# Kernel tuning notes

Measured on AMD Instinct MI355X. Metric: run time of the kernel, lower is better.

Reference implementation:

```python
import jax, jax.numpy as jnp
import numpy as np

B, N, M, D, NHEAD, FF, C, K = 2, 16384, 2048, 256, 8, 512, 50, 3
HID = 128          # embed/pos hidden
HEAD_HID = 256     # seg head hidden
L = 4              # depth
EPS = 1e-5


def setup_inputs() -> dict:
    key = jax.random.key(0)
    ks = jax.random.split(key, 32)
    g = lambda i, shape: jax.random.normal(ks[i], shape, dtype=jnp.float32) * 0.02
    z = lambda shape: jnp.zeros(shape, jnp.float32)
    o = lambda shape: jnp.ones(shape, jnp.float32)
    return {
        "xyz": jax.random.normal(ks[0], (B, N, 3), dtype=jnp.float32),
        "embed_w1": g(1, (3, HID)), "embed_b1": z((HID,)),
        "embed_w2": g(2, (HID, D)), "embed_b2": z((D,)),
        "pos_w1": g(3, (3, HID)), "pos_b1": z((HID,)),
        "pos_w2": g(4, (HID, D)), "pos_b2": z((D,)),
        "Wq": g(5, (L, D, D)), "bq": z((L, D)),
        "Wk": g(6, (L, D, D)), "bk": z((L, D)),
        "Wv": g(7, (L, D, D)), "bv": z((L, D)),
        "Wo": g(8, (L, D, D)), "bo": z((L, D)),
        "ln1_s": o((L, D)), "ln1_b": z((L, D)),
        "W1": g(9, (L, D, FF)), "b1": z((L, FF)),
        "W2": g(10, (L, FF, D)), "b2": z((L, D)),
        "ln2_s": o((L, D)), "ln2_b": z((L, D)),
        "head_w1": g(11, (D, HEAD_HID)), "head_b1": z((HEAD_HID,)),
        "head_w2": g(12, (HEAD_HID, C)), "head_b2": z((C,)),
    }


def _ln(x, s, b):
    m = x.mean(-1, keepdims=True)
    v = ((x - m) ** 2).mean(-1, keepdims=True)
    return (x - m) / jnp.sqrt(v + EPS) * s + b


def reference(xyz, embed_w1, embed_b1, embed_w2, embed_b2,
              pos_w1, pos_b1, pos_w2, pos_b2,
              Wq, bq, Wk, bk, Wv, bv, Wo, bo, ln1_s, ln1_b,
              W1, b1, W2, b2, ln2_s, ln2_b,
              head_w1, head_b1, head_w2, head_b2):
    # deterministic token subsample (replaces randperm stub): strided pick of M points
    stride = N // M
    tok = xyz[:, ::stride, :][:, :M]                                  # [B,M,3]
    # per-point embed + learned positional encoding
    x = jax.nn.relu(tok @ embed_w1 + embed_b1) @ embed_w2 + embed_b2  # [B,M,D]
    x = x + jax.nn.relu(tok @ pos_w1 + pos_b1) @ pos_w2 + pos_b2
    dh = D // NHEAD
    scale = 1.0 / jnp.sqrt(jnp.float32(dh))

    def layer(x, p):
        wq, bq_, wk, bk_, wv, bv_, wo, bo_, l1s, l1b, w1, b1_, w2, b2_, l2s, l2b = p
        # pre-norm MHSA
        y = _ln(x, l1s, l1b)
        q = (y @ wq + bq_).reshape(B, M, NHEAD, dh)
        k = (y @ wk + bk_).reshape(B, M, NHEAD, dh)
        v = (y @ wv + bv_).reshape(B, M, NHEAD, dh)
        att = jax.nn.softmax(jnp.einsum('bqhd,bkhd->bhqk', q, k) * scale, axis=-1)
        o = jnp.einsum('bhqk,bkhd->bqhd', att, v).reshape(B, M, D)
        x = x + o @ wo + bo_
        # pre-norm FFN (gelu, exact erf as in torch)
        y = _ln(x, l2s, l2b)
        x = x + jax.nn.gelu(y @ w1 + b1_, approximate=False) @ w2 + b2_
        return x, None

    x, _ = jax.lax.scan(layer, x, (Wq, bq, Wk, bk, Wv, bv, Wo, bo,
                                   ln1_s, ln1_b, W1, b1, W2, b2, ln2_s, ln2_b))
    logits_tok = jax.nn.relu(x @ head_w1 + head_b1) @ head_w2 + head_b2  # [B,M,C]

    # kNN propagation N->M: dist^2 = |q|^2 + |k|^2 - 2 q.k, topk smallest
    q2 = (xyz ** 2).sum(-1)[..., None]            # [B,N,1]
    k2 = (tok ** 2).sum(-1)[:, None, :]           # [B,1,M]
    dist = q2 + k2 - 2.0 * jnp.einsum('bnd,bmd->bnm', xyz, tok)
    dist = jax.lax.stop_gradient(jnp.maximum(dist, 0.0))
    idx = jax.lax.top_k(-dist, K)[1]              # [B,N,K]
    logits_nk = logits_tok[jnp.arange(B)[:, None, None], idx]  # [B,N,K,C]
    return logits_nk.mean(axis=2)                 # [B,N,C]
```

## Files before the change

### kernel.cpp

```cpp
#include <hip/hip_runtime.h>
#include <hip/hip_bf16.h>
#include <math.h>

#define B_ 2
#define N_ 16384
#define M_ 2048
#define D_ 256
#define NHEAD_ 8
#define DH_ 32
#define FF_ 512
#define C_ 50
#define HID_ 128
#define HHID_ 256
#define L_ 4
#define EPS_ 1e-5f
#define TOK_ (B_*M_)
#define QSCALE_ 0.25507604155757994f

typedef short short8 __attribute__((ext_vector_type(8)));
typedef float f32x4 __attribute__((ext_vector_type(4)));

__device__ __forceinline__ short f2bf(float f) {
  union { float f; unsigned u; } c; c.f = f;
  unsigned u = c.u;
  unsigned r = (u + 0x7FFFu + ((u >> 16) & 1u)) >> 16;
  return (short)r;
}
__device__ __forceinline__ unsigned pack2bf(float a, float b) {
  return ((unsigned)(unsigned short)f2bf(a)) | (((unsigned)(unsigned short)f2bf(b)) << 16);
}
__device__ __forceinline__ float fast_exp2(float x) {
  float r;
  asm("v_exp_f32 %0, %1" : "=v"(r) : "v"(x));
  return r;
}
__device__ __forceinline__ unsigned cvt_pk_bf16(float lo, float hi) {
  unsigned r;
  asm("v_cvt_pk_bf16_f32 %0, %1, %2" : "=v"(r) : "v"(lo), "v"(hi));
  return r;
}

__global__ __launch_bounds__(128) void embed_kernel(
    const float* __restrict__ xyz,
    const float* __restrict__ ew1, const float* __restrict__ eb1,
    const float* __restrict__ ew2, const float* __restrict__ eb2,
    const float* __restrict__ pw1, const float* __restrict__ pb1,
    const float* __restrict__ pw2, const float* __restrict__ pb2,
    float* __restrict__ x) {
  int t = blockIdx.x;
  int b = t / M_, m = t % M_;
  const float* p = xyz + ((size_t)b * N_ + (size_t)m * 8) * 3;
  float t0 = p[0], t1 = p[1], t2 = p[2];
  __shared__ float he[HID_], hp[HID_];
  int j = threadIdx.x;
  {
    float a = fmaf(t0, ew1[j], fmaf(t1, ew1[HID_ + j], fmaf(t2, ew1[2 * HID_ + j], eb1[j])));
    he[j] = fmaxf(a, 0.f);
    float c = fmaf(t0, pw1[j], fmaf(t1, pw1[HID_ + j], fmaf(t2, pw1[2 * HID_ + j], pb1[j])));
    hp[j] = fmaxf(c, 0.f);
  }
  __syncthreads();
  for (int d = j; d < D_; d += HID_) {
    float acc = eb2[d] + pb2[d];
    for (int k = 0; k < HID_; ++k) {
      acc = fmaf(he[k], ew2[k * D_ + d], acc);
      acc = fmaf(hp[k], pw2[k * D_ + d], acc);
    }
    x[(size_t)t * D_ + d] = acc;
  }
}

__global__ __launch_bounds__(256) void ln_kernel(
    const float* __restrict__ x, const float* __restrict__ s,
    const float* __restrict__ bb, float* __restrict__ y) {
  int r = blockIdx.x * 4 + (threadIdx.x >> 6);
  int t = threadIdx.x & 63;
  const float4* xr = (const float4*)(x + (size_t)r * D_);
  float4 v = xr[t];
  float sum = v.x + v.y + v.z + v.w;
  #pragma unroll
  for (int o = 1; o < 64; o <<= 1) sum += __shfl_xor(sum, o, 64);
  float mean = sum * (1.f / D_);
  float dx = v.x - mean, dy = v.y - mean, dz = v.z - mean, dw = v.w - mean;
  float vs = dx * dx + dy * dy + dz * dz + dw * dw;
  #pragma unroll
  for (int o = 1; o < 64; o <<= 1) vs += __shfl_xor(vs, o, 64);
  float inv = 1.0f / sqrtf(vs * (1.f / D_) + EPS_);
  float4 sv = ((const float4*)s)[t];
  float4 bv = ((const float4*)bb)[t];
  float4 out;
  out.x = dx * inv * sv.x + bv.x;
  out.y = dy * inv * sv.y + bv.y;
  out.z = dz * inv * sv.z + bv.z;
  out.w = dw * inv * sv.w + bv.w;
  ((float4*)(y + (size_t)r * D_))[t] = out;
}

template <int ACT, int RES>
__global__ __launch_bounds__(256) void gemm_kernel(
    const float* __restrict__ A, const float* __restrict__ W,
    const float* __restrict__ bias, const float* __restrict__ R,
    float* __restrict__ Cc, int K, int Ncols) {
  __shared__ float As[16][68];
  __shared__ float Ws[16][68];
  int m0 = blockIdx.y * 64;
  int n0 = blockIdx.x * 64;
  int tid = threadIdx.x;
  int tx = tid & 15, ty = tid >> 4;
  float acc[4][4] = {};
  for (int kk = 0; kk < K; kk += 16) {
    for (int i = tid; i < 64 * 16; i += 256) {
      int mm = i >> 4, kq = i & 15;
      As[kq][mm] = A[(size_t)(m0 + mm) * K + kk + kq];
    }
    for (int i = tid; i < 16 * 64; i += 256) {
      int kq = i >> 6, nn = i & 63;
      int n = n0 + nn;
      Ws[kq][nn] = (n < Ncols) ? W[(size_t)(kk + kq) * Ncols + n] : 0.f;
    }
    __syncthreads();
    #pragma unroll
    for (int kq = 0; kq < 16; ++kq) {
      float a[4], w[4];
      #pragma unroll
      for (int i = 0; i < 4; ++i) a[i] = As[kq][ty * 4 + i];
      #pragma unroll
      for (int jj = 0; jj < 4; ++jj) w[jj] = Ws[kq][tx * 4 + jj];
      #pragma unroll
      for (int i = 0; i < 4; ++i)
        #pragma unroll
        for (int jj = 0; jj < 4; ++jj) acc[i][jj] = fmaf(a[i], w[jj], acc[i][jj]);
    }
    __syncthreads();
  }
  #pragma unroll
  for (int i = 0; i < 4; ++i) {
    int m = m0 + ty * 4 + i;
    #pragma unroll
    for (int jj = 0; jj < 4; ++jj) {
      int n = n0 + tx * 4 + jj;
      if (n >= Ncols) continue;
      float v = acc[i][jj] + bias[n];
      if (ACT == 1) v = fmaxf(v, 0.f);
      else if (ACT == 2) v = 0.5f * v * (1.f + erff(v * 0.70710678118654752f));
      if (RES) v += R[(size_t)m * Ncols + n];
      Cc[(size_t)m * Ncols + n] = v;
    }
  }
}

template <int ACT, int RES>
__device__ __forceinline__ void gemm_body(
    const float* __restrict__ A, const float* __restrict__ W,
    const float* __restrict__ bias, const float* __restrict__ R,
    float* __restrict__ Cc, short* __restrict__ out16, float oscale,
    int K, int Ncols, int m0, int n0) {
  __shared__ short As[32][40];
  __shared__ short Bs[64][40];
  int tid = threadIdx.x;
  int w = tid >> 6, l = tid & 63;
  int lq = l & 15, lg = l >> 4;
  int wr = (w & 1) * 16, wc = (w >> 1) * 32;
  int ar = tid >> 3, ak = (tid & 7) * 4;
  int wn = tid & 63, wk = (tid >> 6) * 8;
  f32x4 acc0 = {0.f, 0.f, 0.f, 0.f};
  f32x4 acc1 = {0.f, 0.f, 0.f, 0.f};
  for (int kk = 0; kk < K; kk += 32) {
    __syncthreads();
    {
      float4 a4 = *(const float4*)(A + (size_t)(m0 + ar) * K + kk + ak);
      uint2 au;
      au.x = pack2bf(a4.x, a4.y);
      au.y = pack2bf(a4.z, a4.w);
      *(uint2*)&As[ar][ak] = au;
      const float* wp = W + (size_t)(kk + wk) * Ncols + n0 + wn;
      float w0 = wp[0];
      float w1 = wp[(size_t)Ncols];
      float w2 = wp[2 * (size_t)Ncols];
      float w3 = wp[3 * (size_t)Ncols];
      float w4 = wp[4 * (size_t)Ncols];
      float w5 = wp[5 * (size_t)Ncols];
      float w6 = wp[6 * (size_t)Ncols];
      float w7 = wp[7 * (size_t)Ncols];
      uint4 wu;
      wu.x = pack2bf(w0, w1); wu.y = pack2bf(w2, w3);
      wu.z = pack2bf(w4, w5); wu.w = pack2bf(w6, w7);
      *(uint4*)&Bs[wn][wk] = wu;
    }
    __syncthreads();
    short8 af = *(short8*)&As[wr + lq][lg * 8];
    short8 b0 = *(short8*)&Bs[wc + lq][lg * 8];
    short8 b1 = *(short8*)&Bs[wc + 16 + lq][lg * 8];
    acc0 = __builtin_amdgcn_mfma_f32_16x16x32_bf16(af, b0, acc0, 0, 0, 0);
    acc1 = __builtin_amdgcn_mfma_f32_16x16x32_bf16(af, b1, acc1, 0, 0, 0);
  }
  int row = m0 + wr + lg * 4;
  #pragma unroll
  for (int r = 0; r < 4; ++r) {
    #pragma unroll
    for (int fj = 0; fj < 2; ++fj) {
      int col = n0 + wc + fj * 16 + lq;
      float v = (fj ? acc1[r] : acc0[r]) + bias[col];
      if (ACT == 1) v = fmaxf(v, 0.f);
      else if (ACT == 2) v = 0.5f * v * (1.f + erff(v * 0.70710678118654752f));
      if (RES) v += R[(size_t)(row + r) * Ncols + col];
      if (out16) out16[(size_t)(row + r) * Ncols + col] = f2bf(v * oscale);
      else Cc[(size_t)(row + r) * Ncols + col] = v;
    }
  }
}

template <int ACT, int RES>
__global__ __launch_bounds__(256) void gemm_mfma(
    const float* __restrict__ A, const float* __restrict__ W,
    const float* __restrict__ bias, const float* __restrict__ R,
    float* __restrict__ Cc, int K, int Ncols) {
  gemm_body<ACT, RES>(A, W, bias, R, Cc, nullptr, 1.f, K, Ncols, blockIdx.y * 32, blockIdx.x * 64);
}

__global__ __launch_bounds__(256) void qkv_mfma(
    const float* __restrict__ A,
    const float* __restrict__ Wq, const float* __restrict__ Wk, const float* __restrict__ Wv,
    const float* __restrict__ bq, const float* __restrict__ bk, const float* __restrict__ bv,
    short* __restrict__ q16, short* __restrict__ k16, float* __restrict__ vb) {
  int sel = blockIdx.x >> 2;
  int n0 = (blockIdx.x & 3) << 6;
  const float* W = sel == 0 ? Wq : (sel == 1 ? Wk : Wv);
  const float* bb = sel == 0 ? bq : (sel == 1 ? bk : bv);
  short* out16 = sel == 0 ? q16 : (sel == 1 ? k16 : nullptr);
  float oscale = sel == 0 ? QSCALE_ : 1.f;
  gemm_body<0, 0>(A, W, bb, nullptr, vb, out16, oscale, D_, D_, blockIdx.y * 32, n0);
}

__global__ __launch_bounds__(256) void vtrans_kernel(
    const float* __restrict__ vb, short* __restrict__ vt16) {
  int bid = blockIdx.x;
  int mt = bid & 31;
  int h = (bid >> 5) & 7;
  int b = bid >> 8;
  __shared__ short ts[64][34];
  int m0 = mt * 64;
  int tid = threadIdx.x;
  int mm = tid >> 2, dd = (tid & 3) * 8;
  const float* vp = vb + (size_t)(b * M_ + m0 + mm) * D_ + h * DH_ + dd;
  float4 a0 = ((const float4*)vp)[0];
  float4 a1 = ((const float4*)vp)[1];
  ts[mm][dd + 0] = f2bf(a0.x); ts[mm][dd + 1] = f2bf(a0.y);
  ts[mm][dd + 2] = f2bf(a0.z); ts[mm][dd + 3] = f2bf(a0.w);
  ts[mm][dd + 4] = f2bf(a1.x); ts[mm][dd + 5] = f2bf(a1.y);
  ts[mm][dd + 6] = f2bf(a1.z); ts[mm][dd + 7] = f2bf(a1.w);
  __syncthreads();
  int d = tid >> 3, mc = (tid & 7) * 8;
  short8 r;
  #pragma unroll
  for (int j = 0; j < 8; ++j) r[j] = ts[mc + j][d];
  *(short8*)&vt16[(size_t)((b * NHEAD_ + h) * DH_ + d) * M_ + m0 + mc] = r;
}

#define KSTR 40
#define VSTR 72
#define PSTR 72
__global__ __launch_bounds__(256) void attn_mfma_kernel(
    const short* __restrict__ q16, const short* __restrict__ k16,
    const short* __restrict__ vt16, float* __restrict__ po, float* __restrict__ pl) {
  __shared__ short Ks[64][KSTR];
  __shared__ short Vt[32][VSTR];
  __shared__ short Ps[4][16][PSTR];
  int bid = blockIdx.x;
  int half = bid & 1;
  int qt = (bid >> 1) & 31;
  int h  = (bid >> 6) & 7;
  int b  = bid >> 9;
  int tid = threadIdx.x;
  int w  = tid >> 6;
  int l  = tid & 63;
  int lq = l & 15;
  int lg = l >> 4;

  short8 qf = *(const short8*)&q16[(size_t)(b * M_ + qt * 64 + w * 16 + lq) * D_ + h * DH_ + lg * 8];

  float l_i = 0.f;
  f32x4 o0 = {0.f, 0.f, 0.f, 0.f};
  f32x4 o1 = {0.f, 0.f, 0.f, 0.f};
  int srow = tid >> 2, scol = (tid & 3) * 8;
  int vd = tid >> 3, vm = (tid & 7) * 8;
  const short* kp = k16 + (size_t)(b * M_ + half * 1024 + srow) * D_ + h * DH_ + scol;
  const short* vp = vt16 + (size_t)((b * NHEAD_ + h) * DH_ + vd) * M_ + half * 1024 + vm;

  for (int kt = 0; kt < 16; ++kt) {
    __syncthreads();
    *(short8*)&Ks[srow][scol] = *(const short8*)(kp + (size_t)(kt * 64) * D_);
    *(short8*)&Vt[vd][vm]     = *(const short8*)(vp + kt * 64);
    __syncthreads();
    f32x4 st[4];
    #pragma unroll
    for (int t = 0; t < 4; ++t) {
      short8 kf = *(short8*)&Ks[t * 16 + lq][lg * 8];
      f32x4 z = {0.f, 0.f, 0.f, 0.f};
      st[t] = __builtin_amdgcn_mfma_f32_16x16x32_bf16(kf, qf, z, 0, 0, 0);
    }
    #pragma unroll
    for (int t = 0; t < 4; ++t)
      #pragma unroll
      for (int r2 = 0; r2 < 4; ++r2) {
        st[t][r2] = fast_exp2(st[t][r2]);
        l_i += st[t][r2];
      }
    {
      unsigned* pw = (unsigned*)&Ps[w][lq][0];
      #pragma unroll
      for (int t = 0; t < 4; ++t) {
        uint2 pk;
        pk.x = cvt_pk_bf16(st[t][0], st[t][1]);
        pk.y = cvt_pk_bf16(st[t][2], st[t][3]);
        *(uint2*)(pw + t * 8 + lg * 2) = pk;
      }
    }
    #pragma unroll
    for (int c = 0; c < 2; ++c) {
      short8 pf = *(short8*)&Ps[w][lq][c * 32 + lg * 8];
      short8 v0 = *(short8*)&Vt[lq][c * 32 + lg * 8];
      short8 v1 = *(short8*)&Vt[16 + lq][c * 32 + lg * 8];
      o0 = __builtin_amdgcn_mfma_f32_16x16x32_bf16(v0, pf, o0, 0, 0, 0);
      o1 = __builtin_amdgcn_mfma_f32_16x16x32_bf16(v1, pf, o1, 0, 0, 0);
    }
  }
  l_i += __shfl_xor(l_i, 16, 64);
  l_i += __shfl_xor(l_i, 32, 64);
  int f = (b * NHEAD_ + h) * M_ + qt * 64 + w * 16 + lq;
  float* pp = po + ((size_t)half * (16 * M_) + f) * 32;
  #pragma unroll
  for (int r2 = 0; r2 < 4; ++r2) pp[lg * 4 + r2] = o0[r2];
  #pragma unroll
  for (int r2 = 0; r2 < 4; ++r2) pp[16 + lg * 4 + r2] = o1[r2];
  if (lg == 0) pl[half * (16 * M_) + f] = l_i;
}

__global__ __launch_bounds__(256) void attn_combine(
    const float* __restrict__ po, const float* __restrict__ pl,
    float* __restrict__ o) {
  int idx = blockIdx.x * 256 + threadIdx.x;
  int f = idx >> 3, dq = (idx & 7) * 4;
  float inv = 1.f / (pl[f] + pl[16 * M_ + f]);
  const float4 a = *(const float4*)&po[(size_t)f * 32 + dq];
  const float4 c = *(const float4*)&po[(size_t)(16 * M_ + f) * 32 + dq];
  int b = f >> 14, h = (f >> 11) & 7, m = f & (M_ - 1);
  float4 r;
  r.x = (a.x + c.x) * inv;
  r.y = (a.y + c.y) * inv;
  r.z = (a.z + c.z) * inv;
  r.w = (a.w + c.w) * inv;
  *(float4*)&o[(size_t)(b * M_ + m) * D_ + h * DH_ + dq] = r;
}

__global__ __launch_bounds__(512) void knn_kernel(
    const float* __restrict__ xyz, const float* __restrict__ lt,
    float* __restrict__ out) {
  __shared__ float4 tok[2056];
  int b = blockIdx.x >> 8;
  int q0 = (blockIdx.x & 255) << 6;
  int tid = threadIdx.x;
  for (int i = tid; i < M_; i += 512) {
    const float* tp = xyz + ((size_t)b * N_ + (size_t)i * 8) * 3;
    float a = tp[0], bb = tp[1], cc = tp[2];
    tok[i + (i >> 8)] = make_float4(a, bb, cc, a * a + bb * bb + cc * cc);
  }
  __syncthreads();
  int qi = tid >> 3, sl = tid & 7;
  int n = q0 + qi;
  const float* qp = xyz + ((size_t)b * N_ + n) * 3;
  float qx = qp[0], qy = qp[1], qz = qp[2];
  float q2 = qx * qx + qy * qy + qz * qz;
  float dd0 = INFINITY, dd1 = INFINITY, dd2 = INFINITY;
  int ii0 = 0, ii1 = 0, ii2 = 0;
  const float4* cp = &tok[sl * 257];
  int mb = sl << 8;
  #pragma unroll 4
  for (int j = 0; j < 256; ++j) {
    float4 t = cp[j];
    float dot = fmaf(qx, t.x, fmaf(qy, t.y, qz * t.z));
    float d = fmaxf(q2 + t.w - 2.f * dot, 0.f);
    if (d < dd2) {
      int m = mb + j;
      if (d < dd1) {
        dd2 = dd1; ii2 = ii1;
        if (d < dd0) { dd1 = dd0; ii1 = ii0; dd0 = d; ii0 = m; }
        else         { dd1 = d;  ii1 = m; }
      } else         { dd2 = d;  ii2 = m; }
    }
  }
  auto insT = [&](float d, int i) {
    if (d < dd2 || (d == dd2 && i < ii2)) {
      if (d < dd1 || (d == dd1 && i < ii1)) {
        dd2 = dd1; ii2 = ii1;
        if (d < dd0 || (d == dd0 && i < ii0)) { dd1 = dd0; ii1 = ii0; dd0 = d; ii0 = i; }
        else { dd1 = d; ii1 = i; }
      } else { dd2 = d; ii2 = i; }
    }
  };
  #pragma unroll
  for (int off = 1; off < 8; off <<= 1) {
    float pd0 = __shfl_xor(dd0, off, 64); int pi0 = __shfl_xor(ii0, off, 64);
    float pd1 = __shfl_xor(dd1, off, 64); int pi1 = __shfl_xor(ii1, off, 64);
    float pd2 = __shfl_xor(dd2, off, 64); int pi2 = __shfl_xor(ii2, off, 64);
    insT(pd0, pi0); insT(pd1, pi1); insT(pd2, pi2);
  }
  const float* l0 = lt + ((size_t)b * M_ + ii0) * C_;
  const float* l1 = lt + ((size_t)b * M_ + ii1) * C_;
  const float* l2 = lt + ((size_t)b * M_ + ii2) * C_;
  float* op = out + ((size_t)b * N_ + n) * C_;
  for (int cc = sl; cc < C_; cc += 8)
    op[cc] = (l0[cc] + l1[cc] + l2[cc]) * (1.f / 3.f);
}

extern "C" void kernel_launch(void* const* d_in, const int* in_sizes, int n_in,
                              void* d_out, int out_size, void* d_ws, size_t ws_size,
                              hipStream_t stream) {
  const float* xyz  = (const float*)d_in[0];
  const float* ew1  = (const float*)d_in[1];
  const float* eb1  = (const float*)d_in[2];
  const float* ew2  = (const float*)d_in[3];
  const float* eb2  = (const float*)d_in[4];
  const float* pw1  = (const float*)d_in[5];
  const float* pb1  = (const float*)d_in[6];
  const float* pw2  = (const float*)d_in[7];
  const float* pb2  = (const float*)d_in[8];
  const float* Wq   = (const float*)d_in[9];
  const float* bq   = (const float*)d_in[10];
  const float* Wk   = (const float*)d_in[11];
  const float* bk   = (const float*)d_in[12];
  const float* Wv   = (const float*)d_in[13];
  const float* bv   = (const float*)d_in[14];
  const float* Wo   = (const float*)d_in[15];
  const float* bo   = (const float*)d_in[16];
  const float* ln1s = (const float*)d_in[17];
  const float* ln1b = (const float*)d_in[18];
  const float* W1   = (const float*)d_in[19];
  const float* b1   = (const float*)d_in[20];
  const float* W2   = (const float*)d_in[21];
  const float* b2   = (const float*)d_in[22];
  const float* ln2s = (const float*)d_in[23];
  const float* ln2b = (const float*)d_in[24];
  const float* hw1  = (const float*)d_in[25];
  const float* hb1  = (const float*)d_in[26];
  const float* hw2  = (const float*)d_in[27];
  const float* hb2  = (const float*)d_in[28];
  float* out = (float*)d_out;

  float* x  = (float*)d_ws;
  float* y  = x  + (size_t)TOK_ * D_;
  float* qb = y  + (size_t)TOK_ * D_;
  float* kb = qb + (size_t)TOK_ * D_;
  float* vb = kb + (size_t)TOK_ * D_;
  float* ob = vb + (size_t)TOK_ * D_;
  float* ff = ob + (size_t)TOK_ * D_;
  float* lt = ff + (size_t)TOK_ * FF_;

  short* qb16 = (short*)qb;
  short* kb16 = qb16 + (size_t)TOK_ * D_;
  short* vt16 = (short*)kb;
  float* po = ff;
  float* pl = lt;

  embed_kernel<<<TOK_, 128, 0, stream>>>(xyz, ew1, eb1, ew2, eb2, pw1, pb1, pw2, pb2, x);

  dim3 gQKV(12, TOK_ / 32);
  dim3 gD(D_ / 64, TOK_ / 32);
  dim3 gF(FF_ / 64, TOK_ / 32);
  for (int l = 0; l < L_; ++l) {
    const float* wq = Wq + (size_t)l * D_ * D_;
    const float* wk = Wk + (size_t)l * D_ * D_;
    const float* wv = Wv + (size_t)l * D_ * D_;
    const float* wo = Wo + (size_t)l * D_ * D_;
    ln_kernel<<<TOK_ / 4, 256, 0, stream>>>(x, ln1s + l * D_, ln1b + l * D_, y);
    qkv_mfma<<<gQKV, 256, 0, stream>>>(y, wq, wk, wv, bq + l * D_, bk + l * D_, bv + l * D_, qb16, kb16, vb);
    vtrans_kernel<<<512, 256, 0, stream>>>(vb, vt16);
    attn_mfma_kernel<<<1024, 256, 0, stream>>>(qb16, kb16, vt16, po, pl);
    attn_combine<<<1024, 256, 0, stream>>>(po, pl, ob);
    gemm_mfma<0, 1><<<gD, 256, 0, stream>>>(ob, wo, bo + l * D_, x, x, D_, D_);
    ln_kernel<<<TOK_ / 4, 256, 0, stream>>>(x, ln2s + l * D_, ln2b + l * D_, y);
    gemm_mfma<2, 0><<<gF, 256, 0, stream>>>(y, W1 + (size_t)l * D_ * FF_, b1 + l * FF_, nullptr, ff, D_, FF_);
    gemm_mfma<0, 1><<<gD, 256, 0, stream>>>(ff, W2 + (size_t)l * FF_ * D_, b2 + l * D_, x, x, FF_, D_);
  }
  gemm_mfma<1, 0><<<dim3(HHID_ / 64, TOK_ / 32), 256, 0, stream>>>(x, hw1, hb1, nullptr, y, D_, HHID_);
  gemm_kernel<0, 0><<<dim3(1, TOK_ / 64), 256, 0, stream>>>(y, hw2, hb2, nullptr, lt, HHID_, C_);
  knn_kernel<<<512, 512, 0, stream>>>(xyz, lt, out);
}
```

Before: 436.6 us.

## Split attention keys into four partitions and add dedicated head2 kernel

```diff
diff --git a/kernel.cpp b/kernel.cpp
--- a/kernel.cpp
+++ b/kernel.cpp
@@ -96,57 +96,24 @@
   ((float4*)(y + (size_t)r * D_))[t] = out;
 }
 
-template <int ACT, int RES>
-__global__ __launch_bounds__(256) void gemm_kernel(
-    const float* __restrict__ A, const float* __restrict__ W,
-    const float* __restrict__ bias, const float* __restrict__ R,
-    float* __restrict__ Cc, int K, int Ncols) {
-  __shared__ float As[16][68];
-  __shared__ float Ws[16][68];
-  int m0 = blockIdx.y * 64;
-  int n0 = blockIdx.x * 64;
-  int tid = threadIdx.x;
-  int tx = tid & 15, ty = tid >> 4;
-  float acc[4][4] = {};
-  for (int kk = 0; kk < K; kk += 16) {
-    for (int i = tid; i < 64 * 16; i += 256) {
-      int mm = i >> 4, kq = i & 15;
-      As[kq][mm] = A[(size_t)(m0 + mm) * K + kk + kq];
-    }
-    for (int i = tid; i < 16 * 64; i += 256) {
-      int kq = i >> 6, nn = i & 63;
-      int n = n0 + nn;
-      Ws[kq][nn] = (n < Ncols) ? W[(size_t)(kk + kq) * Ncols + n] : 0.f;
-    }
-    __syncthreads();
-    #pragma unroll
-    for (int kq = 0; kq < 16; ++kq) {
-      float a[4], w[4];
-      #pragma unroll
-      for (int i = 0; i < 4; ++i) a[i] = As[kq][ty * 4 + i];
-      #pragma unroll
-      for (int jj = 0; jj < 4; ++jj) w[jj] = Ws[kq][tx * 4 + jj];
-      #pragma unroll
-      for (int i = 0; i < 4; ++i)
-        #pragma unroll
-        for (int jj = 0; jj < 4; ++jj) acc[i][jj] = fmaf(a[i], w[jj], acc[i][jj]);
-    }
-    __syncthreads();
-  }
-  #pragma unroll
-  for (int i = 0; i < 4; ++i) {
-    int m = m0 + ty * 4 + i;
-    #pragma unroll
-    for (int jj = 0; jj < 4; ++jj) {
-      int n = n0 + tx * 4 + jj;
-      if (n >= Ncols) continue;
-      float v = acc[i][jj] + bias[n];
-      if (ACT == 1) v = fmaxf(v, 0.f);
-      else if (ACT == 2) v = 0.5f * v * (1.f + erff(v * 0.70710678118654752f));
-      if (RES) v += R[(size_t)m * Ncols + n];
-      Cc[(size_t)m * Ncols + n] = v;
-    }
-  }
+__global__ __launch_bounds__(256) void head2_kernel(
+    const float* __restrict__ y, const float* __restrict__ w2,
+    const float* __restrict__ b2, float* __restrict__ lt) {
+  __shared__ float ys[4][HHID_];
+  int w = threadIdx.x >> 6, l = threadIdx.x & 63;
+  int t = blockIdx.x * 4 + w;
+  float4 v = ((const float4*)(y + (size_t)t * HHID_))[l];
+  *(float4*)&ys[w][l * 4] = v;
+  int c = l < C_ ? l : 0;
+  float a0 = 0.f, a1 = 0.f, a2 = 0.f, a3 = 0.f;
+  #pragma unroll 4
+  for (int k = 0; k < HHID_; k += 4) {
+    a0 = fmaf(ys[w][k + 0], w2[(k + 0) * C_ + c], a0);
+    a1 = fmaf(ys[w][k + 1], w2[(k + 1) * C_ + c], a1);
+    a2 = fmaf(ys[w][k + 2], w2[(k + 2) * C_ + c], a2);
+    a3 = fmaf(ys[w][k + 3], w2[(k + 3) * C_ + c], a3);
+  }
+  if (l < C_) lt[(size_t)t * C_ + l] = (a0 + a1) + (a2 + a3) + b2[l];
 }
 
 template <int ACT, int RES>
@@ -262,15 +229,18 @@
 #define PSTR 72
 __global__ __launch_bounds__(256) void attn_mfma_kernel(
     const short* __restrict__ q16, const short* __restrict__ k16,
-    const short* __restrict__ vt16, float* __restrict__ po, float* __restrict__ pl) {
+    const short* __restrict__ vt16,
+    float* __restrict__ po0, float* __restrict__ po1,
+    float* __restrict__ po2, float* __restrict__ po3,
+    float* __restrict__ pl) {
   __shared__ short Ks[64][KSTR];
   __shared__ short Vt[32][VSTR];
   __shared__ short Ps[4][16][PSTR];
   int bid = blockIdx.x;
-  int half = bid & 1;
-  int qt = (bid >> 1) & 31;
-  int h  = (bid >> 6) & 7;
-  int b  = bid >> 9;
+  int quar = bid & 3;
+  int qt = (bid >> 2) & 31;
+  int h  = (bid >> 7) & 7;
+  int b  = bid >> 10;
   int tid = threadIdx.x;
   int w  = tid >> 6;
   int l  = tid & 63;
@@ -284,10 +254,10 @@
   f32x4 o1 = {0.f, 0.f, 0.f, 0.f};
   int srow = tid >> 2, scol = (tid & 3) * 8;
   int vd = tid >> 3, vm = (tid & 7) * 8;
-  const short* kp = k16 + (size_t)(b * M_ + half * 1024 + srow) * D_ + h * DH_ + scol;
-  const short* vp = vt16 + (size_t)((b * NHEAD_ + h) * DH_ + vd) * M_ + half * 1024 + vm;
-
-  for (int kt = 0; kt < 16; ++kt) {
+  const short* kp = k16 + (size_t)(b * M_ + quar * 512 + srow) * D_ + h * DH_ + scol;
+  const short* vp = vt16 + (size_t)((b * NHEAD_ + h) * DH_ + vd) * M_ + quar * 512 + vm;
+
+  for (int kt = 0; kt < 8; ++kt) {
     __syncthreads();
     *(short8*)&Ks[srow][scol] = *(const short8*)(kp + (size_t)(kt * 64) * D_);
     *(short8*)&Vt[vd][vm]     = *(const short8*)(vp + kt * 64);
@@ -328,28 +298,31 @@
   l_i += __shfl_xor(l_i, 16, 64);
   l_i += __shfl_xor(l_i, 32, 64);
   int f = (b * NHEAD_ + h) * M_ + qt * 64 + w * 16 + lq;
-  float* pp = po + ((size_t)half * (16 * M_) + f) * 32;
+  float* pp = (quar == 0 ? po0 : quar == 1 ? po1 : quar == 2 ? po2 : po3) + (size_t)f * 32;
   #pragma unroll
   for (int r2 = 0; r2 < 4; ++r2) pp[lg * 4 + r2] = o0[r2];
   #pragma unroll
   for (int r2 = 0; r2 < 4; ++r2) pp[16 + lg * 4 + r2] = o1[r2];
-  if (lg == 0) pl[half * (16 * M_) + f] = l_i;
+  if (lg == 0) pl[quar * (16 * M_) + f] = l_i;
 }
 
 __global__ __launch_bounds__(256) void attn_combine(
-    const float* __restrict__ po, const float* __restrict__ pl,
-    float* __restrict__ o) {
+    const float* __restrict__ po0, const float* __restrict__ po1,
+    const float* __restrict__ po2, const float* __restrict__ po3,
+    const float* __restrict__ pl, float* __restrict__ o) {
   int idx = blockIdx.x * 256 + threadIdx.x;
   int f = idx >> 3, dq = (idx & 7) * 4;
-  float inv = 1.f / (pl[f] + pl[16 * M_ + f]);
-  const float4 a = *(const float4*)&po[(size_t)f * 32 + dq];
-  const float4 c = *(const float4*)&po[(size_t)(16 * M_ + f) * 32 + dq];
+  float inv = 1.f / (pl[f] + pl[16 * M_ + f] + pl[32 * M_ + f] + pl[48 * M_ + f]);
+  const float4 a = *(const float4*)&po0[(size_t)f * 32 + dq];
+  const float4 c = *(const float4*)&po1[(size_t)f * 32 + dq];
+  const float4 e = *(const float4*)&po2[(size_t)f * 32 + dq];
+  const float4 g = *(const float4*)&po3[(size_t)f * 32 + dq];
   int b = f >> 14, h = (f >> 11) & 7, m = f & (M_ - 1);
   float4 r;
-  r.x = (a.x + c.x) * inv;
-  r.y = (a.y + c.y) * inv;
-  r.z = (a.z + c.z) * inv;
-  r.w = (a.w + c.w) * inv;
+  r.x = (a.x + c.x + e.x + g.x) * inv;
+  r.y = (a.y + c.y + e.y + g.y) * inv;
+  r.z = (a.z + c.z + e.z + g.z) * inv;
+  r.w = (a.w + c.w + e.w + g.w) * inv;
   *(float4*)&o[(size_t)(b * M_ + m) * D_ + h * DH_ + dq] = r;
 }
 
@@ -459,7 +432,10 @@
   short* qb16 = (short*)qb;
   short* kb16 = qb16 + (size_t)TOK_ * D_;
   short* vt16 = (short*)kb;
-  float* po = ff;
+  float* po0 = y;
+  float* po1 = vb;
+  float* po2 = ff;
+  float* po3 = ff + (size_t)TOK_ * D_;
   float* pl = lt;
 
   embed_kernel<<<TOK_, 128, 0, stream>>>(xyz, ew1, eb1, ew2, eb2, pw1, pb1, pw2, pb2, x);
@@ -475,14 +451,14 @@
     ln_kernel<<<TOK_ / 4, 256, 0, stream>>>(x, ln1s + l * D_, ln1b + l * D_, y);
     qkv_mfma<<<gQKV, 256, 0, stream>>>(y, wq, wk, wv, bq + l * D_, bk + l * D_, bv + l * D_, qb16, kb16, vb);
     vtrans_kernel<<<512, 256, 0, stream>>>(vb, vt16);
-    attn_mfma_kernel<<<1024, 256, 0, stream>>>(qb16, kb16, vt16, po, pl);
-    attn_combine<<<1024, 256, 0, stream>>>(po, pl, ob);
+    attn_mfma_kernel<<<2048, 256, 0, stream>>>(qb16, kb16, vt16, po0, po1, po2, po3, pl);
+    attn_combine<<<1024, 256, 0, stream>>>(po0, po1, po2, po3, pl, ob);
     gemm_mfma<0, 1><<<gD, 256, 0, stream>>>(ob, wo, bo + l * D_, x, x, D_, D_);
     ln_kernel<<<TOK_ / 4, 256, 0, stream>>>(x, ln2s + l * D_, ln2b + l * D_, y);
     gemm_mfma<2, 0><<<gF, 256, 0, stream>>>(y, W1 + (size_t)l * D_ * FF_, b1 + l * FF_, nullptr, ff, D_, FF_);
     gemm_mfma<0, 1><<<gD, 256, 0, stream>>>(ff, W2 + (size_t)l * FF_ * D_, b2 + l * D_, x, x, FF_, D_);
   }
   gemm_mfma<1, 0><<<dim3(HHID_ / 64, TOK_ / 32), 256, 0, stream>>>(x, hw1, hb1, nullptr, y, D_, HHID_);
-  gemm_kernel<0, 0><<<dim3(1, TOK_ / 64), 256, 0, stream>>>(y, hw2, hb2, nullptr, lt, HHID_, C_);
+  head2_kernel<<<TOK_ / 4, 256, 0, stream>>>(y, hw2, hb2, lt);
   knn_kernel<<<512, 512, 0, stream>>>(xyz, lt, out);
 }
```

Result: faster. 415.7 us (-4.8%).
